# Kernel optimization log

Measured on AMD Instinct MI355X. Metric: run time of the kernel, lower is better.

The kernel has to match this reference:

```python
import jax, jax.numpy as jnp
import numpy as np


def _graph_conv(feat, W, b, src, dst, num_nodes):
    """DGL GraphConv with norm='both', activation=relu.
    out = relu(D_in^{-1/2} * A * D_out^{-1/2} * (X @ W) + b)
    Degrees are clamped to a minimum of 1 (DGL behavior).
    """
    # Linear transform first (d_in == d_out here, order is math-equivalent)
    h = feat @ W  # [N, d_out]
    ones = jnp.ones(src.shape[0], dtype=feat.dtype)
    out_deg = jnp.clip(jax.ops.segment_sum(ones, src, num_segments=num_nodes), 1.0)
    in_deg = jnp.clip(jax.ops.segment_sum(ones, dst, num_segments=num_nodes), 1.0)
    norm_src = jax.lax.rsqrt(out_deg)  # [N]
    norm_dst = jax.lax.rsqrt(in_deg)   # [N]
    # gather messages from source nodes, scaled by src norm
    msg = h[src] * norm_src[src][:, None]  # [E, d_out]
    agg = jax.ops.segment_sum(msg, dst, num_segments=num_nodes)  # [N, d_out]
    return jax.nn.relu(agg * norm_dst[:, None] + b)


def setup_inputs() -> dict:
    key = jax.random.key(0)
    ks = jax.random.split(key, 8)
    N = 50000
    E_c, E_d = 1600000, 800000
    d_c, d_d = 128, 256
    feat_c = jax.random.normal(ks[0], (N, d_c), dtype=jnp.float32)
    feat_d = jax.random.normal(ks[1], (N, d_d), dtype=jnp.float32)
    src_c = jax.random.randint(ks[2], (E_c,), 0, N, dtype=jnp.int32)
    dst_c = jax.random.randint(ks[3], (E_c,), 0, N, dtype=jnp.int32)
    src_d = jax.random.randint(ks[4], (E_d,), 0, N, dtype=jnp.int32)
    dst_d = jax.random.randint(ks[5], (E_d,), 0, N, dtype=jnp.int32)
    W_c = jax.random.normal(ks[6], (d_c, d_c), dtype=jnp.float32) * (1.0 / np.sqrt(d_c))
    W_d = jax.random.normal(ks[7], (d_d, d_d), dtype=jnp.float32) * (1.0 / np.sqrt(d_d))
    b_c = jnp.zeros((d_c,), dtype=jnp.float32)
    b_d = jnp.zeros((d_d,), dtype=jnp.float32)
    return {"feat_c": feat_c, "feat_d": feat_d, "src_c": src_c, "dst_c": dst_c,
            "src_d": src_d, "dst_d": dst_d, "W_c": W_c, "b_c": b_c,
            "W_d": W_d, "b_d": b_d}


def reference(feat_c, feat_d, src_c, dst_c, src_d, dst_d, W_c, b_c, W_d, b_d):
    N_c = feat_c.shape[0]
    N_d = feat_d.shape[0]
    homo_feature_c = _graph_conv(feat_c, W_c, b_c, src_c, dst_c, N_c)
    homo_feature_d = _graph_conv(feat_d, W_d, b_d, src_d, dst_d, N_d)
    return (homo_feature_c, homo_feature_d)
```

## Files before the change

### kernel.cpp

```cpp
#include <hip/hip_runtime.h>
#include <hip/hip_bf16.h>


typedef __attribute__((ext_vector_type(8))) short short8;
typedef __attribute__((ext_vector_type(4))) float f32x4;

#define RND 4096
#define CAPMAX 8960

static __device__ __forceinline__ ushort f2b(float f) {
    __hip_bfloat16 h = __float2bfloat16(f);
    return *reinterpret_cast<ushort*>(&h);
}
static __device__ __forceinline__ float b2f(ushort u) {
    union { unsigned int i; float f; } c;
    c.i = ((unsigned int)u) << 16;
    return c.f;
}
static __device__ __forceinline__ void gld_lds16(const void* g, void* l) {
    __builtin_amdgcn_global_load_lds(
        (const __attribute__((address_space(1))) unsigned int*)g,
        (__attribute__((address_space(3))) unsigned int*)l, 16, 0, 0);
}

__global__ __launch_bounds__(256) void part_kernel(
    const int* __restrict__ src_c, const int* __restrict__ dst_c, int Ec, int Rc,
    const int* __restrict__ src_d, const int* __restrict__ dst_d, int Ed, int Rd,
    int* gf_cd, int* gf_cs, int* gf_dd, int* gf_ds,
    int* dbuf_c, int* sbuf_c, int* dbuf_d, int* sbuf_d, int capc, int capd)
{
    __shared__ int pk[RND];
    __shared__ unsigned char pb[RND];
    __shared__ int hist[256], st[256], ex2[256], cur[256], gbase[256];

    const int tid = threadIdx.x;
    const int bid = blockIdx.x;
    const int* keys; const int* pays; int E; int* gf; int* buf; int cap; int e0;
    if (bid < Rc)            { keys = dst_c; pays = src_c; E = Ec; gf = gf_cd; buf = dbuf_c; cap = capc; e0 = bid * RND; }
    else if (bid < 2 * Rc)   { keys = src_c; pays = 0;     E = Ec; gf = gf_cs; buf = sbuf_c; cap = capc; e0 = (bid - Rc) * RND; }
    else if (bid < 2 * Rc + Rd) { keys = dst_d; pays = src_d; E = Ed; gf = gf_dd; buf = dbuf_d; cap = capd; e0 = (bid - 2 * Rc) * RND; }
    else                     { keys = src_d; pays = 0;     E = Ed; gf = gf_ds; buf = sbuf_d; cap = capd; e0 = (bid - 2 * Rc - Rd) * RND; }

    hist[tid] = 0;
    __syncthreads();

    int kb[RND / 256], pv[RND / 256];
    int n = 0;
#pragma unroll
    for (int r = 0; r < RND / 256; ++r) {
        int e = e0 + r * 256 + tid;
        if (e < E) {
            int k = keys[e];
            pv[r] = pays ? ((pays[e] << 8) | (k & 255)) : k;
            kb[r] = k >> 8;
            atomicAdd(&hist[kb[r]], 1);
            n = r + 1;
        }
    }
    __syncthreads();

    int x = hist[tid];
    st[tid] = x;
    __syncthreads();
    for (int off = 1; off < 256; off <<= 1) {
        int t2 = 0;
        if (tid >= off) t2 = st[tid - off];
        __syncthreads();
        if (tid >= off) st[tid] += t2;
        __syncthreads();
    }
    ex2[tid] = st[tid] - x;
    cur[tid] = st[tid] - x;
    __syncthreads();

    for (int r = 0; r < n; ++r) {
        int slot = atomicAdd(&cur[kb[r]], 1);
        pk[slot] = pv[r];
        pb[slot] = (unsigned char)kb[r];
    }
    if (x) gbase[tid] = atomicAdd(&gf[tid], x);
    __syncthreads();

    int m = st[255];
    for (int i = tid; i < m; i += 256) {
        int b = pb[i];
        int pos = gbase[b] + (i - ex2[b]);
        if (pos < cap) buf[(size_t)b * cap + pos] = pk[i];
    }
}

__global__ __launch_bounds__(256) void b2s_kernel(
    const int* __restrict__ sbuf_c, const int* __restrict__ gf_cs, int capc, int* cnt_c,
    const int* __restrict__ sbuf_d, const int* __restrict__ gf_ds, int capd, int* cnt_d,
    int N, int NBKT)
{
    __shared__ int h[256];
    const int tid = threadIdx.x;
    const int* sbuf; const int* gf; int cap; int* cnt; int bb;
    if ((int)blockIdx.x < NBKT) { sbuf = sbuf_c; gf = gf_cs; cap = capc; cnt = cnt_c; bb = blockIdx.x; }
    else { sbuf = sbuf_d; gf = gf_ds; cap = capd; cnt = cnt_d; bb = blockIdx.x - NBKT; }
    h[tid] = 0;
    __syncthreads();
    int m = gf[bb]; if (m > cap) m = cap;
    const int* reg = sbuf + (size_t)bb * cap;
    for (int i = tid; i < m; i += 256) atomicAdd(&h[reg[i] & 255], 1);
    __syncthreads();
    int v = bb * 256 + tid;
    if (v < N) cnt[v] = h[tid];
}

__global__ __launch_bounds__(256) void b2d_kernel(
    int* dbuf_c, const int* __restrict__ gf_cd, int capc, int* rs_c, int* dg_c,
    int* dbuf_d, const int* __restrict__ gf_dd, int capd, int* rs_d, int* dg_d,
    int N, int NBKT)
{
    __shared__ int pk[CAPMAX];
    __shared__ int h[256], st[256], ex2[256], cur[256];
    const int tid = threadIdx.x;
    int* bbuf; const int* gf; int cap; int* rs; int* dg; int bb;
    if ((int)blockIdx.x < NBKT) { bbuf = dbuf_c; gf = gf_cd; cap = capc; rs = rs_c; dg = dg_c; bb = blockIdx.x; }
    else { bbuf = dbuf_d; gf = gf_dd; cap = capd; rs = rs_d; dg = dg_d; bb = blockIdx.x - NBKT; }

    int m = gf[bb]; if (m > cap) m = cap;
    int* reg = bbuf + (size_t)bb * cap;

    h[tid] = 0;
    __syncthreads();
    for (int i = tid; i < m; i += 256) atomicAdd(&h[reg[i] & 255], 1);
    __syncthreads();
    int x = h[tid];
    st[tid] = x;
    __syncthreads();
    for (int off = 1; off < 256; off <<= 1) {
        int t2 = 0;
        if (tid >= off) t2 = st[tid - off];
        __syncthreads();
        if (tid >= off) st[tid] += t2;
        __syncthreads();
    }
    int ex_t = st[tid] - x;
    ex2[tid] = ex_t;
    cur[tid] = ex_t;
    int v = bb * 256 + tid;
    if (v < N) { rs[v] = bb * cap + ex_t; dg[v] = x; }
    __syncthreads();
    for (int i = tid; i < m; i += 256) {
        int p = reg[i];
        int slot = atomicAdd(&cur[p & 255], 1);
        pk[slot] = p >> 8;
    }
    __syncthreads();
    for (int i = tid; i < m; i += 256) reg[i] = pk[i];
}

__global__ __launch_bounds__(256) void wprep_kernel(
    const float* __restrict__ Wc, const float* __restrict__ Wd,
    ushort* __restrict__ Wtc, ushort* __restrict__ Wtd)
{
    int t = blockIdx.x * 256 + threadIdx.x;
    const float* W; ushort* Wt; int BN, tile, idx;
    if (t < 2048)        { W = Wc; Wt = Wtc; BN = 128; tile = t >> 10; idx = t & 1023; }
    else if (t < 10240)  { int tt = t - 2048; W = Wd; Wt = Wtd; BN = 256; tile = tt >> 10; idx = tt & 1023; }
    else return;
    int np = idx >> 3, slot = idx & 7;
    int ch = tile >> 2, ci = tile & 3;
    int k0 = ci * 64 + ((slot ^ (np & 7)) << 3);
    int ncol = ch * 128 + np;
    ushort o[8];
#pragma unroll
    for (int j = 0; j < 8; ++j) o[j] = f2b(W[(size_t)(k0 + j) * BN + ncol]);
    uint4 vv;
    vv.x = (unsigned)o[0] | ((unsigned)o[1] << 16);
    vv.y = (unsigned)o[2] | ((unsigned)o[3] << 16);
    vv.z = (unsigned)o[4] | ((unsigned)o[5] << 16);
    vv.w = (unsigned)o[6] | ((unsigned)o[7] << 16);
    *(uint4*)&Wt[tile * 8192 + np * 64 + slot * 8] = vv;
}

__global__ __launch_bounds__(256) void cast_kernel(
    const float* __restrict__ Xc, const int* __restrict__ coc, ushort* __restrict__ Xbc,
    const float* __restrict__ Xd, const int* __restrict__ cod, ushort* __restrict__ Xbd,
    int N, int nbc)
{
    const float* X; const int* co; ushort* Xb; int C4, t;
    if ((int)blockIdx.x < nbc) { X = Xc; co = coc; Xb = Xbc; C4 = 32; t = blockIdx.x * 256 + threadIdx.x; }
    else { X = Xd; co = cod; Xb = Xbd; C4 = 64; t = (blockIdx.x - nbc) * 256 + threadIdx.x; }
    if (t >= N * C4) return;
    int row = t / C4, c4 = t % C4;
    int od = co[row]; if (od < 1) od = 1;
    float nr = rsqrtf((float)od);
    float4 xv = ((const float4*)(X + (size_t)row * (C4 * 4)))[c4];
    ushort4 o;
    o.x = f2b(xv.x * nr); o.y = f2b(xv.y * nr);
    o.z = f2b(xv.z * nr); o.w = f2b(xv.w * nr);
    ((ushort4*)(Xb + (size_t)row * (C4 * 4)))[c4] = o;
}

template <int VEC>
static __device__ __forceinline__ void fused_branch(
    int blk, const ushort* __restrict__ Xb, const int* __restrict__ rs,
    const int* __restrict__ dg, const int* __restrict__ csr,
    const ushort* __restrict__ Wt, const float* __restrict__ bias,
    float* __restrict__ out, int N, ushort* At, ushort* Wls)
{
    constexpr int D = VEC * 64;
    constexpr int CH = VEC / 2;
    constexpr int KCH = VEC;
    const int tid = threadIdx.x;
    const int lane = tid & 63, wid = tid >> 6;

#pragma unroll
    for (int it = 0; it < 2; ++it) {
        int off16 = it * 512 + tid;
        gld_lds16(&Wt[off16 * 8], &Wls[off16 * 8]);
    }

    const int node0 = blk * 32;
#pragma unroll
    for (int s = 0; s < 4; ++s) {
        const int row = wid * 4 + s;
        const int v = node0 + row;
        float acc[VEC];
#pragma unroll
        for (int k = 0; k < VEC; ++k) acc[k] = 0.f;
        int deg = 0;
        if (v < N) {
            deg = dg[v];
            const int* rowp = csr + rs[v];
            for (int base = 0; base < deg; base += 64) {
                int m = deg - base; if (m > 64) m = 64;
                int u_l = (lane < m) ? rowp[base + lane] : 0;
#pragma unroll 8
                for (int j = 0; j < m; ++j) {
                    int u = __shfl(u_l, j);
                    const ushort* xr = Xb + (size_t)u * D + lane * VEC;
                    if constexpr (VEC == 2) {
                        unsigned int xv = *(const unsigned int*)xr;
                        acc[0] += b2f((ushort)(xv & 0xffff));
                        acc[1] += b2f((ushort)(xv >> 16));
                    } else {
                        uint2 xv = *(const uint2*)xr;
                        acc[0] += b2f((ushort)(xv.x & 0xffff));
                        acc[1] += b2f((ushort)(xv.x >> 16));
                        acc[2] += b2f((ushort)(xv.y & 0xffff));
                        acc[3] += b2f((ushort)(xv.y >> 16));
                    }
                }
            }
        }
        float nd = rsqrtf((float)(deg < 1 ? 1 : deg));
        const int k0 = lane * VEC;
        const int slot = (k0 >> 3) ^ (row & 7);
        ushort* dstp = &At[row * D + slot * 8 + (k0 & 7)];
        if constexpr (VEC == 2) {
            unsigned int pk = (unsigned)f2b(acc[0] * nd) | ((unsigned)f2b(acc[1] * nd) << 16);
            *(unsigned int*)dstp = pk;
        } else {
            uint2 pk;
            pk.x = (unsigned)f2b(acc[0] * nd) | ((unsigned)f2b(acc[1] * nd) << 16);
            pk.y = (unsigned)f2b(acc[2] * nd) | ((unsigned)f2b(acc[3] * nd) << 16);
            *(uint2*)dstp = pk;
        }
    }
    __syncthreads();

    const int wr = wid >> 2, wc = wid & 3;
    const int lr = lane & 15, lk8 = (lane >> 4) * 8;
    f32x4 acc[CH][2];
#pragma unroll
    for (int ch = 0; ch < CH; ++ch)
#pragma unroll
        for (int nc = 0; nc < 2; ++nc) acc[ch][nc] = (f32x4)0.f;

#pragma unroll
    for (int ch = 0; ch < CH; ++ch) {
#pragma unroll
        for (int ci = 0; ci < KCH; ++ci) {
            const int tile = ch * KCH + ci;
            if (tile) {
                __syncthreads();
#pragma unroll
                for (int it = 0; it < 2; ++it) {
                    int off16 = it * 512 + tid;
                    gld_lds16(&Wt[tile * 8192 + off16 * 8], &Wls[off16 * 8]);
                }
                __syncthreads();
            }
#pragma unroll
            for (int k0 = 0; k0 < 64; k0 += 32) {
                const int r = wr * 16 + lr;
                const int kg = ci * 64 + k0 + lk8;
                const int aslot = (kg >> 3) ^ (r & 7);
                short8 a = *(const short8*)&At[r * D + aslot * 8];
#pragma unroll
                for (int nc = 0; nc < 2; ++nc) {
                    const int np = wc * 32 + nc * 16 + lr;
                    const int kk = k0 + lk8;
                    const int bslot = (kk >> 3) ^ (np & 7);
                    short8 b = *(const short8*)&Wls[np * 64 + bslot * 8];
                    acc[ch][nc] = __builtin_amdgcn_mfma_f32_16x16x32_bf16(a, b, acc[ch][nc], 0, 0, 0);
                }
            }
        }
    }

#pragma unroll
    for (int ch = 0; ch < CH; ++ch)
#pragma unroll
        for (int nc = 0; nc < 2; ++nc) {
            const int col = ch * 128 + wc * 32 + nc * 16 + lr;
            const float bv = bias[col];
#pragma unroll
            for (int r4 = 0; r4 < 4; ++r4) {
                const int row = wr * 16 + (lane >> 4) * 4 + r4;
                const int v = node0 + row;
                if (v < N)
                    out[(size_t)v * D + col] = fmaxf(acc[ch][nc][r4] + bv, 0.f);
            }
        }
}

__global__ __launch_bounds__(512) void fused_kernel(
    const ushort* __restrict__ Xbc, const int* __restrict__ rsc,
    const int* __restrict__ dgc, const int* __restrict__ csrc,
    const ushort* __restrict__ Wtc, const float* __restrict__ bc, float* outc,
    const ushort* __restrict__ Xbd, const int* __restrict__ rsd,
    const int* __restrict__ dgd, const int* __restrict__ csrd,
    const ushort* __restrict__ Wtd, const float* __restrict__ bd, float* outd,
    int N, int nblkc)
{
    __shared__ ushort At[32 * 256];
    __shared__ ushort Wls[8192];
    if ((int)blockIdx.x < nblkc)
        fused_branch<2>(blockIdx.x, Xbc, rsc, dgc, csrc, Wtc, bc, outc, N, At, Wls);
    else
        fused_branch<4>(blockIdx.x - nblkc, Xbd, rsd, dgd, csrd, Wtd, bd, outd, N, At, Wls);
}

extern "C" void kernel_launch(void* const* d_in, const int* in_sizes, int n_in,
                              void* d_out, int out_size, void* d_ws, size_t ws_size,
                              hipStream_t stream)
{
    const float* feat_c = (const float*)d_in[0];
    const float* feat_d = (const float*)d_in[1];
    const int* src_c = (const int*)d_in[2];
    const int* dst_c = (const int*)d_in[3];
    const int* src_d = (const int*)d_in[4];
    const int* dst_d = (const int*)d_in[5];
    const float* W_c = (const float*)d_in[6];
    const float* b_c = (const float*)d_in[7];
    const float* W_d = (const float*)d_in[8];
    const float* b_d = (const float*)d_in[9];

    const int D_c = in_sizes[7];
    const int D_d = in_sizes[9];
    const int N = in_sizes[0] / D_c;
    const int E_c = in_sizes[2];
    const int E_d = in_sizes[4];

    float* out_c = (float*)d_out;
    float* out_d = (float*)d_out + (size_t)N * D_c;

    const int NBKT = (N + 255) >> 8;
    int capc = E_c / NBKT; capc += 8 * (int)sqrtf((float)capc) + 32; capc = (capc + 15) & ~15;
    int capd = E_d / NBKT; capd += 8 * (int)sqrtf((float)capd) + 32; capd = (capd + 15) & ~15;
    if (capc > CAPMAX) capc = CAPMAX;
    if (capd > CAPMAX) capd = CAPMAX;

    int* ws = (int*)d_ws;
    int* cnt_out_c = ws;
    int* cnt_out_d = ws + N;
    int* gf_cd = ws + 2 * (size_t)N;
    int* gf_cs = gf_cd + 256;
    int* gf_dd = gf_cs + 256;
    int* gf_ds = gf_dd + 256;
    int* rs_c  = gf_ds + 256;
    int* dg_c  = rs_c + N;
    int* rs_d  = dg_c + N;
    int* dg_d  = rs_d + N;
    ushort* Wt_c = (ushort*)(dg_d + N);
    ushort* Wt_d = Wt_c + 16384;
    int* dbuf_c = (int*)(Wt_d + 65536);
    int* sbuf_c = dbuf_c + (size_t)NBKT * capc;
    int* dbuf_d = sbuf_c + (size_t)NBKT * capc;
    int* sbuf_d = dbuf_d + (size_t)NBKT * capd;
    ushort* Xb_c = (ushort*)(sbuf_d + (size_t)NBKT * capd);
    ushort* Xb_d = Xb_c + (size_t)N * D_c;

    hipMemsetAsync(gf_cd, 0, 1024 * sizeof(int), stream);

    wprep_kernel<<<40, 256, 0, stream>>>(W_c, W_d, Wt_c, Wt_d);

    const int Rc = (E_c + RND - 1) / RND;
    const int Rd = (E_d + RND - 1) / RND;
    part_kernel<<<2 * (Rc + Rd), 256, 0, stream>>>(
        src_c, dst_c, E_c, Rc, src_d, dst_d, E_d, Rd,
        gf_cd, gf_cs, gf_dd, gf_ds,
        dbuf_c, sbuf_c, dbuf_d, sbuf_d, capc, capd);

    b2s_kernel<<<2 * NBKT, 256, 0, stream>>>(
        sbuf_c, gf_cs, capc, cnt_out_c,
        sbuf_d, gf_ds, capd, cnt_out_d, N, NBKT);

    int nbc = (N * (D_c / 4) + 255) / 256, nbd = (N * (D_d / 4) + 255) / 256;
    cast_kernel<<<nbc + nbd, 256, 0, stream>>>(feat_c, cnt_out_c, Xb_c,
                                               feat_d, cnt_out_d, Xb_d, N, nbc);

    b2d_kernel<<<2 * NBKT, 256, 0, stream>>>(
        dbuf_c, gf_cd, capc, rs_c, dg_c,
        dbuf_d, gf_dd, capd, rs_d, dg_d, N, NBKT);

    const int nblk = (N + 31) / 32;
    fused_kernel<<<2 * nblk, 512, 0, stream>>>(
        Xb_c, rs_c, dg_c, dbuf_c, Wt_c, b_c, out_c,
        Xb_d, rs_d, dg_d, dbuf_d, Wt_d, b_d, out_d, N, nblk);
}
```

Baseline: 402.7 us.

## Merge partition passes, shrink source buckets to bytes, fuse bucket kernels

The partition kernel now reads src/dst once per block and performs both the destination and source bucketing in the same block. Source bucket entries are stored as single bytes instead of ints, which cuts the write and read traffic for degree counting. The source-count and destination-CSR bucket kernels are merged into one launch, and the memset is folded into the weight-prep kernel to remove launches. The fused kernel interleaves c/d branch blocks and preloads degree and row-start values, trading extra register pressure for less launch overhead and better mixing of blocks.

```diff
diff --git a/kernel.cpp b/kernel.cpp
--- a/kernel.cpp
+++ b/kernel.cpp
@@ -6,6 +6,7 @@
 typedef __attribute__((ext_vector_type(4))) float f32x4;
 
 #define RND 4096
+#define EPT (RND / 256)
 #define CAPMAX 8960
 
 static __device__ __forceinline__ ushort f2b(float f) {
@@ -23,11 +24,26 @@
         (__attribute__((address_space(3))) unsigned int*)l, 16, 0, 0);
 }
 
+static __device__ __forceinline__ int scan_ex(int x, int* st, int tid, int* total) {
+    st[tid] = x;
+    __syncthreads();
+    for (int off = 1; off < 256; off <<= 1) {
+        int t2 = 0;
+        if (tid >= off) t2 = st[tid - off];
+        __syncthreads();
+        if (tid >= off) st[tid] += t2;
+        __syncthreads();
+    }
+    *total = st[255];
+    return st[tid] - x;
+}
+
 __global__ __launch_bounds__(256) void part_kernel(
     const int* __restrict__ src_c, const int* __restrict__ dst_c, int Ec, int Rc,
-    const int* __restrict__ src_d, const int* __restrict__ dst_d, int Ed, int Rd,
+    const int* __restrict__ src_d, const int* __restrict__ dst_d, int Ed,
     int* gf_cd, int* gf_cs, int* gf_dd, int* gf_ds,
-    int* dbuf_c, int* sbuf_c, int* dbuf_d, int* sbuf_d, int capc, int capd)
+    int* dbuf_c, unsigned char* sbuf_c, int* dbuf_d, unsigned char* sbuf_d,
+    int capc, int capd)
 {
     __shared__ int pk[RND];
     __shared__ unsigned char pb[RND];
@@ -35,91 +51,115 @@
 
     const int tid = threadIdx.x;
     const int bid = blockIdx.x;
-    const int* keys; const int* pays; int E; int* gf; int* buf; int cap; int e0;
-    if (bid < Rc)            { keys = dst_c; pays = src_c; E = Ec; gf = gf_cd; buf = dbuf_c; cap = capc; e0 = bid * RND; }
-    else if (bid < 2 * Rc)   { keys = src_c; pays = 0;     E = Ec; gf = gf_cs; buf = sbuf_c; cap = capc; e0 = (bid - Rc) * RND; }
-    else if (bid < 2 * Rc + Rd) { keys = dst_d; pays = src_d; E = Ed; gf = gf_dd; buf = dbuf_d; cap = capd; e0 = (bid - 2 * Rc) * RND; }
-    else                     { keys = src_d; pays = 0;     E = Ed; gf = gf_ds; buf = sbuf_d; cap = capd; e0 = (bid - 2 * Rc - Rd) * RND; }
-
+    const int* src; const int* dst; int E; int* gfd; int* gfs;
+    int* dbuf; unsigned char* sbuf; int cap; int e0;
+    if (bid < Rc) { src = src_c; dst = dst_c; E = Ec; gfd = gf_cd; gfs = gf_cs;
+                    dbuf = dbuf_c; sbuf = sbuf_c; cap = capc; e0 = bid * RND; }
+    else          { src = src_d; dst = dst_d; E = Ed; gfd = gf_dd; gfs = gf_ds;
+                    dbuf = dbuf_d; sbuf = sbuf_d; cap = capd; e0 = (bid - Rc) * RND; }
+
+    int sv[EPT], dv[EPT];
     hist[tid] = 0;
     __syncthreads();
-
-    int kb[RND / 256], pv[RND / 256];
-    int n = 0;
-#pragma unroll
-    for (int r = 0; r < RND / 256; ++r) {
+#pragma unroll
+    for (int r = 0; r < EPT; ++r) {
         int e = e0 + r * 256 + tid;
-        if (e < E) {
-            int k = keys[e];
-            pv[r] = pays ? ((pays[e] << 8) | (k & 255)) : k;
-            kb[r] = k >> 8;
-            atomicAdd(&hist[kb[r]], 1);
-            n = r + 1;
-        }
-    }
-    __syncthreads();
-
-    int x = hist[tid];
-    st[tid] = x;
-    __syncthreads();
-    for (int off = 1; off < 256; off <<= 1) {
-        int t2 = 0;
-        if (tid >= off) t2 = st[tid - off];
-        __syncthreads();
-        if (tid >= off) st[tid] += t2;
-        __syncthreads();
-    }
-    ex2[tid] = st[tid] - x;
-    cur[tid] = st[tid] - x;
-    __syncthreads();
-
-    for (int r = 0; r < n; ++r) {
-        int slot = atomicAdd(&cur[kb[r]], 1);
-        pk[slot] = pv[r];
-        pb[slot] = (unsigned char)kb[r];
-    }
-    if (x) gbase[tid] = atomicAdd(&gf[tid], x);
-    __syncthreads();
-
-    int m = st[255];
-    for (int i = tid; i < m; i += 256) {
-        int b = pb[i];
-        int pos = gbase[b] + (i - ex2[b]);
-        if (pos < cap) buf[(size_t)b * cap + pos] = pk[i];
-    }
-}
-
-__global__ __launch_bounds__(256) void b2s_kernel(
-    const int* __restrict__ sbuf_c, const int* __restrict__ gf_cs, int capc, int* cnt_c,
-    const int* __restrict__ sbuf_d, const int* __restrict__ gf_ds, int capd, int* cnt_d,
-    int N, int NBKT)
-{
-    __shared__ int h[256];
-    const int tid = threadIdx.x;
-    const int* sbuf; const int* gf; int cap; int* cnt; int bb;
-    if ((int)blockIdx.x < NBKT) { sbuf = sbuf_c; gf = gf_cs; cap = capc; cnt = cnt_c; bb = blockIdx.x; }
-    else { sbuf = sbuf_d; gf = gf_ds; cap = capd; cnt = cnt_d; bb = blockIdx.x - NBKT; }
-    h[tid] = 0;
-    __syncthreads();
-    int m = gf[bb]; if (m > cap) m = cap;
-    const int* reg = sbuf + (size_t)bb * cap;
-    for (int i = tid; i < m; i += 256) atomicAdd(&h[reg[i] & 255], 1);
-    __syncthreads();
-    int v = bb * 256 + tid;
-    if (v < N) cnt[v] = h[tid];
-}
-
-__global__ __launch_bounds__(256) void b2d_kernel(
+        if (e < E) { sv[r] = src[e]; dv[r] = dst[e]; atomicAdd(&hist[dv[r] >> 8], 1); }
+    }
+    __syncthreads();
+
+    {
+        int x = hist[tid];
+        int tot;
+        int ex = scan_ex(x, st, tid, &tot);
+        ex2[tid] = ex; cur[tid] = ex;
+        __syncthreads();
+#pragma unroll
+        for (int r = 0; r < EPT; ++r) {
+            int e = e0 + r * 256 + tid;
+            if (e < E) {
+                int b = dv[r] >> 8;
+                int slot = atomicAdd(&cur[b], 1);
+                pk[slot] = (sv[r] << 8) | (dv[r] & 255);
+                pb[slot] = (unsigned char)b;
+            }
+        }
+        if (x) gbase[tid] = atomicAdd(&gfd[tid], x);
+        __syncthreads();
+        for (int i = tid; i < tot; i += 256) {
+            int b = pb[i];
+            int pos = gbase[b] + (i - ex2[b]);
+            if (pos < cap) dbuf[(size_t)b * cap + pos] = pk[i];
+        }
+        __syncthreads();
+    }
+
+    hist[tid] = 0;
+    __syncthreads();
+#pragma unroll
+    for (int r = 0; r < EPT; ++r) {
+        int e = e0 + r * 256 + tid;
+        if (e < E) atomicAdd(&hist[sv[r] >> 8], 1);
+    }
+    __syncthreads();
+    {
+        int x = hist[tid];
+        int tot;
+        int ex = scan_ex(x, st, tid, &tot);
+        ex2[tid] = ex; cur[tid] = ex;
+        __syncthreads();
+        unsigned char* pkb = (unsigned char*)pk;
+#pragma unroll
+        for (int r = 0; r < EPT; ++r) {
+            int e = e0 + r * 256 + tid;
+            if (e < E) {
+                int b = sv[r] >> 8;
+                int slot = atomicAdd(&cur[b], 1);
+                pkb[slot] = (unsigned char)(sv[r] & 255);
+                pb[slot] = (unsigned char)b;
+            }
+        }
+        if (x) gbase[tid] = atomicAdd(&gfs[tid], x);
+        __syncthreads();
+        for (int i = tid; i < tot; i += 256) {
+            int b = pb[i];
+            int pos = gbase[b] + (i - ex2[b]);
+            if (pos < cap) sbuf[(size_t)b * cap + pos] = pkb[i];
+        }
+    }
+}
+
+__global__ __launch_bounds__(256) void b2sd_kernel(
     int* dbuf_c, const int* __restrict__ gf_cd, int capc, int* rs_c, int* dg_c,
     int* dbuf_d, const int* __restrict__ gf_dd, int capd, int* rs_d, int* dg_d,
+    const unsigned char* __restrict__ sbuf_c, const int* __restrict__ gf_cs, int* cnt_c,
+    const unsigned char* __restrict__ sbuf_d, const int* __restrict__ gf_ds, int* cnt_d,
     int N, int NBKT)
 {
     __shared__ int pk[CAPMAX];
     __shared__ int h[256], st[256], ex2[256], cur[256];
     const int tid = threadIdx.x;
+    int bid = blockIdx.x;
+
+    if (bid >= 2 * NBKT) {
+        bid -= 2 * NBKT;
+        const unsigned char* sbuf; const int* gf; int cap; int* cnt; int bb;
+        if (bid < NBKT) { sbuf = sbuf_c; gf = gf_cs; cap = capc; cnt = cnt_c; bb = bid; }
+        else { sbuf = sbuf_d; gf = gf_ds; cap = capd; cnt = cnt_d; bb = bid - NBKT; }
+        h[tid] = 0;
+        __syncthreads();
+        int m = gf[bb]; if (m > cap) m = cap;
+        const unsigned char* reg = sbuf + (size_t)bb * cap;
+        for (int i = tid; i < m; i += 256) atomicAdd(&h[reg[i]], 1);
+        __syncthreads();
+        int v = bb * 256 + tid;
+        if (v < N) cnt[v] = h[tid];
+        return;
+    }
+
     int* bbuf; const int* gf; int cap; int* rs; int* dg; int bb;
-    if ((int)blockIdx.x < NBKT) { bbuf = dbuf_c; gf = gf_cd; cap = capc; rs = rs_c; dg = dg_c; bb = blockIdx.x; }
-    else { bbuf = dbuf_d; gf = gf_dd; cap = capd; rs = rs_d; dg = dg_d; bb = blockIdx.x - NBKT; }
+    if (bid < NBKT) { bbuf = dbuf_c; gf = gf_cd; cap = capc; rs = rs_c; dg = dg_c; bb = bid; }
+    else { bbuf = dbuf_d; gf = gf_dd; cap = capd; rs = rs_d; dg = dg_d; bb = bid - NBKT; }
 
     int m = gf[bb]; if (m > cap) m = cap;
     int* reg = bbuf + (size_t)bb * cap;
@@ -129,16 +169,8 @@
     for (int i = tid; i < m; i += 256) atomicAdd(&h[reg[i] & 255], 1);
     __syncthreads();
     int x = h[tid];
-    st[tid] = x;
-    __syncthreads();
-    for (int off = 1; off < 256; off <<= 1) {
-        int t2 = 0;
-        if (tid >= off) t2 = st[tid - off];
-        __syncthreads();
-        if (tid >= off) st[tid] += t2;
-        __syncthreads();
-    }
-    int ex_t = st[tid] - x;
+    int tot;
+    int ex_t = scan_ex(x, st, tid, &tot);
     ex2[tid] = ex_t;
     cur[tid] = ex_t;
     int v = bb * 256 + tid;
@@ -155,13 +187,17 @@
 
 __global__ __launch_bounds__(256) void wprep_kernel(
     const float* __restrict__ Wc, const float* __restrict__ Wd,
-    ushort* __restrict__ Wtc, ushort* __restrict__ Wtd)
+    ushort* __restrict__ Wtc, ushort* __restrict__ Wtd, int* __restrict__ gfz)
 {
     int t = blockIdx.x * 256 + threadIdx.x;
+    if (t >= 10240) {
+        int z = t - 10240;
+        if (z < 1024) gfz[z] = 0;
+        return;
+    }
     const float* W; ushort* Wt; int BN, tile, idx;
-    if (t < 2048)        { W = Wc; Wt = Wtc; BN = 128; tile = t >> 10; idx = t & 1023; }
-    else if (t < 10240)  { int tt = t - 2048; W = Wd; Wt = Wtd; BN = 256; tile = tt >> 10; idx = tt & 1023; }
-    else return;
+    if (t < 2048) { W = Wc; Wt = Wtc; BN = 128; tile = t >> 10; idx = t & 1023; }
+    else { int tt = t - 2048; W = Wd; Wt = Wtd; BN = 256; tile = tt >> 10; idx = tt & 1023; }
     int np = idx >> 3, slot = idx & 7;
     int ch = tile >> 2, ci = tile & 3;
     int k0 = ci * 64 + ((slot ^ (np & 7)) << 3);
@@ -216,35 +252,38 @@
     }
 
     const int node0 = blk * 32;
+    int vdeg[4], vbeg[4];
+#pragma unroll
+    for (int s = 0; s < 4; ++s) {
+        int v = node0 + wid * 4 + s;
+        vdeg[s] = (v < N) ? dg[v] : 0;
+        vbeg[s] = (v < N) ? rs[v] : 0;
+    }
 #pragma unroll
     for (int s = 0; s < 4; ++s) {
         const int row = wid * 4 + s;
-        const int v = node0 + row;
+        const int deg = vdeg[s];
         float acc[VEC];
 #pragma unroll
         for (int k = 0; k < VEC; ++k) acc[k] = 0.f;
-        int deg = 0;
-        if (v < N) {
-            deg = dg[v];
-            const int* rowp = csr + rs[v];
-            for (int base = 0; base < deg; base += 64) {
-                int m = deg - base; if (m > 64) m = 64;
-                int u_l = (lane < m) ? rowp[base + lane] : 0;
+        const int* rowp = csr + vbeg[s];
+        for (int base = 0; base < deg; base += 64) {
+            int m = deg - base; if (m > 64) m = 64;
+            int u_l = (lane < m) ? rowp[base + lane] : 0;
 #pragma unroll 8
-                for (int j = 0; j < m; ++j) {
-                    int u = __shfl(u_l, j);
-                    const ushort* xr = Xb + (size_t)u * D + lane * VEC;
-                    if constexpr (VEC == 2) {
-                        unsigned int xv = *(const unsigned int*)xr;
-                        acc[0] += b2f((ushort)(xv & 0xffff));
-                        acc[1] += b2f((ushort)(xv >> 16));
-                    } else {
-                        uint2 xv = *(const uint2*)xr;
-                        acc[0] += b2f((ushort)(xv.x & 0xffff));
-                        acc[1] += b2f((ushort)(xv.x >> 16));
-                        acc[2] += b2f((ushort)(xv.y & 0xffff));
-                        acc[3] += b2f((ushort)(xv.y >> 16));
-                    }
+            for (int j = 0; j < m; ++j) {
+                int u = __shfl(u_l, j);
+                const ushort* xr = Xb + (size_t)u * D + lane * VEC;
+                if constexpr (VEC == 2) {
+                    unsigned int xv = *(const unsigned int*)xr;
+                    acc[0] += b2f((ushort)(xv & 0xffff));
+                    acc[1] += b2f((ushort)(xv >> 16));
+                } else {
+                    uint2 xv = *(const uint2*)xr;
+                    acc[0] += b2f((ushort)(xv.x & 0xffff));
+                    acc[1] += b2f((ushort)(xv.x >> 16));
+                    acc[2] += b2f((ushort)(xv.y & 0xffff));
+                    acc[3] += b2f((ushort)(xv.y >> 16));
                 }
             }
         }
@@ -253,13 +292,13 @@
         const int slot = (k0 >> 3) ^ (row & 7);
         ushort* dstp = &At[row * D + slot * 8 + (k0 & 7)];
         if constexpr (VEC == 2) {
-            unsigned int pk = (unsigned)f2b(acc[0] * nd) | ((unsigned)f2b(acc[1] * nd) << 16);
-            *(unsigned int*)dstp = pk;
+            unsigned int pkv = (unsigned)f2b(acc[0] * nd) | ((unsigned)f2b(acc[1] * nd) << 16);
+            *(unsigned int*)dstp = pkv;
         } else {
-            uint2 pk;
-            pk.x = (unsigned)f2b(acc[0] * nd) | ((unsigned)f2b(acc[1] * nd) << 16);
-            pk.y = (unsigned)f2b(acc[2] * nd) | ((unsigned)f2b(acc[3] * nd) << 16);
-            *(uint2*)dstp = pk;
+            uint2 pkv;
+            pkv.x = (unsigned)f2b(acc[0] * nd) | ((unsigned)f2b(acc[1] * nd) << 16);
+            pkv.y = (unsigned)f2b(acc[2] * nd) | ((unsigned)f2b(acc[3] * nd) << 16);
+            *(uint2*)dstp = pkv;
         }
     }
     __syncthreads();
@@ -327,14 +366,14 @@
     const ushort* __restrict__ Xbd, const int* __restrict__ rsd,
     const int* __restrict__ dgd, const int* __restrict__ csrd,
     const ushort* __restrict__ Wtd, const float* __restrict__ bd, float* outd,
-    int N, int nblkc)
+    int N)
 {
     __shared__ ushort At[32 * 256];
     __shared__ ushort Wls[8192];
-    if ((int)blockIdx.x < nblkc)
-        fused_branch<2>(blockIdx.x, Xbc, rsc, dgc, csrc, Wtc, bc, outc, N, At, Wls);
+    if (!(blockIdx.x & 1))
+        fused_branch<2>(blockIdx.x >> 1, Xbc, rsc, dgc, csrc, Wtc, bc, outc, N, At, Wls);
     else
-        fused_branch<4>(blockIdx.x - nblkc, Xbd, rsd, dgd, csrd, Wtd, bd, outd, N, At, Wls);
+        fused_branch<4>(blockIdx.x >> 1, Xbd, rsd, dgd, csrd, Wtd, bd, outd, N, At, Wls);
 }
 
 extern "C" void kernel_launch(void* const* d_in, const int* in_sizes, int n_in,
@@ -367,51 +406,46 @@
     if (capc > CAPMAX) capc = CAPMAX;
     if (capd > CAPMAX) capd = CAPMAX;
 
-    int* ws = (int*)d_ws;
-    int* cnt_out_c = ws;
-    int* cnt_out_d = ws + N;
-    int* gf_cd = ws + 2 * (size_t)N;
-    int* gf_cs = gf_cd + 256;
-    int* gf_dd = gf_cs + 256;
-    int* gf_ds = gf_dd + 256;
-    int* rs_c  = gf_ds + 256;
-    int* dg_c  = rs_c + N;
-    int* rs_d  = dg_c + N;
-    int* dg_d  = rs_d + N;
-    ushort* Wt_c = (ushort*)(dg_d + N);
-    ushort* Wt_d = Wt_c + 16384;
-    int* dbuf_c = (int*)(Wt_d + 65536);
-    int* sbuf_c = dbuf_c + (size_t)NBKT * capc;
-    int* dbuf_d = sbuf_c + (size_t)NBKT * capc;
-    int* sbuf_d = dbuf_d + (size_t)NBKT * capd;
-    ushort* Xb_c = (ushort*)(sbuf_d + (size_t)NBKT * capd);
-    ushort* Xb_d = Xb_c + (size_t)N * D_c;
-
-    hipMemsetAsync(gf_cd, 0, 1024 * sizeof(int), stream);
-
-    wprep_kernel<<<40, 256, 0, stream>>>(W_c, W_d, Wt_c, Wt_d);
+    char* p = (char*)d_ws;
+    auto alloc = [&](size_t bytes) { char* r = p; p += (bytes + 15) & ~(size_t)15; return r; };
+    int* cnt_out_c = (int*)alloc((size_t)N * 4);
+    int* cnt_out_d = (int*)alloc((size_t)N * 4);
+    int* gf = (int*)alloc(1024 * 4);
+    int* gf_cd = gf, * gf_cs = gf + 256, * gf_dd = gf + 512, * gf_ds = gf + 768;
+    int* rs_c = (int*)alloc((size_t)N * 4);
+    int* dg_c = (int*)alloc((size_t)N * 4);
+    int* rs_d = (int*)alloc((size_t)N * 4);
+    int* dg_d = (int*)alloc((size_t)N * 4);
+    ushort* Wt_c = (ushort*)alloc(16384 * 2);
+    ushort* Wt_d = (ushort*)alloc(65536 * 2);
+    int* dbuf_c = (int*)alloc((size_t)NBKT * capc * 4);
+    int* dbuf_d = (int*)alloc((size_t)NBKT * capd * 4);
+    unsigned char* sbuf_c = (unsigned char*)alloc((size_t)NBKT * capc);
+    unsigned char* sbuf_d = (unsigned char*)alloc((size_t)NBKT * capd);
+    ushort* Xb_c = (ushort*)alloc((size_t)N * D_c * 2);
+    ushort* Xb_d = (ushort*)alloc((size_t)N * D_d * 2);
+
+    wprep_kernel<<<44, 256, 0, stream>>>(W_c, W_d, Wt_c, Wt_d, gf);
 
     const int Rc = (E_c + RND - 1) / RND;
     const int Rd = (E_d + RND - 1) / RND;
-    part_kernel<<<2 * (Rc + Rd), 256, 0, stream>>>(
-        src_c, dst_c, E_c, Rc, src_d, dst_d, E_d, Rd,
+    part_kernel<<<Rc + Rd, 256, 0, stream>>>(
+        src_c, dst_c, E_c, Rc, src_d, dst_d, E_d,
         gf_cd, gf_cs, gf_dd, gf_ds,
         dbuf_c, sbuf_c, dbuf_d, sbuf_d, capc, capd);
 
-    b2s_kernel<<<2 * NBKT, 256, 0, stream>>>(
-        sbuf_c, gf_cs, capc, cnt_out_c,
-        sbuf_d, gf_ds, capd, cnt_out_d, N, NBKT);
+    b2sd_kernel<<<4 * NBKT, 256, 0, stream>>>(
+        dbuf_c, gf_cd, capc, rs_c, dg_c,
+        dbuf_d, gf_dd, capd, rs_d, dg_d,
+        sbuf_c, gf_cs, cnt_out_c,
+        sbuf_d, gf_ds, cnt_out_d, N, NBKT);
 
     int nbc = (N * (D_c / 4) + 255) / 256, nbd = (N * (D_d / 4) + 255) / 256;
     cast_kernel<<<nbc + nbd, 256, 0, stream>>>(feat_c, cnt_out_c, Xb_c,
                                                feat_d, cnt_out_d, Xb_d, N, nbc);
 
-    b2d_kernel<<<2 * NBKT, 256, 0, stream>>>(
-        dbuf_c, gf_cd, capc, rs_c, dg_c,
-        dbuf_d, gf_dd, capd, rs_d, dg_d, N, NBKT);
-
     const int nblk = (N + 31) / 32;
     fused_kernel<<<2 * nblk, 512, 0, stream>>>(
         Xb_c, rs_c, dg_c, dbuf_c, Wt_c, b_c, out_c,
-        Xb_d, rs_d, dg_d, dbuf_d, Wt_d, b_d, out_d, N, nblk);
-}
+        Xb_d, rs_d, dg_d, dbuf_d, Wt_d, b_d, out_d, N);
+}
```

After: 427.7 us. 1.06x slower.
